# Optimization experiments

Measured on AMD Instinct MI355X. Metric: run time of the kernel, lower is better.

## Reference

```python
import jax, jax.numpy as jnp
import numpy as np

VOCAB = 50257
EMBED = 512
HEADS = 8
HEAD_DIM = EMBED // HEADS
WINDOW = 128
NUM_CLASS = 20
B, S = 4, 2048


def setup_inputs() -> dict:
    key = jax.random.key(0)
    ks = jax.random.split(key, 16)
    sc = 0.02
    inp = {
        'text': jax.random.randint(ks[0], (B, S), 0, VOCAB),
        'emb': jax.random.normal(ks[1], (VOCAB, EMBED), jnp.float32) * sc,
        'in_w': jax.random.normal(ks[2], (3 * EMBED, EMBED), jnp.float32) * sc,
        'in_b': jnp.zeros((3 * EMBED,), jnp.float32),
        'out_w': jax.random.normal(ks[3], (EMBED, EMBED), jnp.float32) * sc,
        'out_b': jnp.zeros((EMBED,), jnp.float32),
        'w1': jax.random.normal(ks[4], (512, EMBED), jnp.float32) * sc,
        'b1': jnp.zeros((512,), jnp.float32),
        'w2': jax.random.normal(ks[5], (256, 512), jnp.float32) * sc,
        'b2': jnp.zeros((256,), jnp.float32),
        'w3': jax.random.normal(ks[6], (128, 256), jnp.float32) * sc,
        'b3': jnp.zeros((128,), jnp.float32),
        'w4': jax.random.normal(ks[7], (NUM_CLASS, 128), jnp.float32) * sc,
        'b4': jnp.zeros((NUM_CLASS,), jnp.float32),
    }
    return inp


def _banded_mask(seq_len, window):
    i = jnp.arange(seq_len)[:, None]
    j = jnp.arange(seq_len)[None, :]
    allowed = jnp.abs(i - j) <= window  # band of width 2*window+1
    return jnp.where(allowed, 0.0, -jnp.inf).astype(jnp.float32)


def reference(text, emb, in_w, in_b, out_w, out_b, w1, b1, w2, b2, w3, b3, w4, b4):
    # Embedding lookup (dropout is identity in eval mode)
    x = emb[text]  # [B, S, E]
    b, s, e = x.shape

    # torch nn.MultiheadAttention: packed in_proj, scaling by 1/sqrt(head_dim)
    wq, wk, wv = in_w[:e], in_w[e:2 * e], in_w[2 * e:]
    bq, bk, bv = in_b[:e], in_b[e:2 * e], in_b[2 * e:]
    q = (x @ wq.T + bq).reshape(b, s, HEADS, HEAD_DIM)
    k = (x @ wk.T + bk).reshape(b, s, HEADS, HEAD_DIM)
    v = (x @ wv.T + bv).reshape(b, s, HEADS, HEAD_DIM)

    mask = _banded_mask(s, WINDOW)  # [S, S] additive, -inf outside band
    scores = jnp.einsum('bihd,bjhd->bhij', q, k) / jnp.sqrt(jnp.float32(HEAD_DIM))
    probs = jax.nn.softmax(scores + mask, axis=-1)  # [B, H, S, S]
    attn = jnp.einsum('bhij,bjhd->bihd', probs, v).reshape(b, s, e)
    attn = attn @ out_w.T + out_b  # [B, S, E]

    # max-pool over sequence
    ctx = jnp.max(attn, axis=1)  # [B, E]

    # MLP head with leaky_relu (negative_slope=0.01, torch default)
    h = jax.nn.leaky_relu(ctx @ w1.T + b1, 0.01)
    h = jax.nn.leaky_relu(h @ w2.T + b2, 0.01)
    h = jax.nn.leaky_relu(h @ w3.T + b3, 0.01)
    return h @ w4.T + b4  # [B, NUM_CLASS]
```

## Files before the change

### kernel.cpp

```cpp
#include <hip/hip_runtime.h>

typedef unsigned short u16;
typedef __attribute__((ext_vector_type(8))) short bf16x8;
typedef __attribute__((ext_vector_type(4))) float f32x4;

#define S_LEN 2048
#define EMBED 512
#define HEADS 8
#define HDIM 64
#define BATCH 4
#define TOKENS (BATCH * S_LEN)

__device__ __forceinline__ u16 f2bf(float f) {
  union { float f; unsigned u; } v;
  v.f = f;
  unsigned r = v.u + 0x7fffu + ((v.u >> 16) & 1u);
  return (u16)(r >> 16);
}

__device__ __forceinline__ void gl2lds16(const void* g, void* l) {
  __builtin_amdgcn_global_load_lds(
      (const __attribute__((address_space(1))) void*)g,
      (__attribute__((address_space(3))) void*)l, 16, 0, 0);
}

__global__ __launch_bounds__(256) void prep_kernel(
    const int* __restrict__ text, const float* __restrict__ emb,
    const float* __restrict__ in_w, const float* __restrict__ out_w,
    u16* __restrict__ Xb, u16* __restrict__ Wq, u16* __restrict__ Wo) {
  const int bid = blockIdx.x;
  const int tid = threadIdx.x;
  if (bid < 4096) {
    const int t = bid * 2 + (tid >> 7);
    const int c = (tid & 127) * 4;
    const size_t src = (size_t)text[t] * EMBED + c;
    const float4 v = *(const float4*)(emb + src);
    u16* dst = Xb + (size_t)t * EMBED + c;
    dst[0] = f2bf(v.x); dst[1] = f2bf(v.y); dst[2] = f2bf(v.z); dst[3] = f2bf(v.w);
  } else {
    const int idx4 = ((bid - 4096) * 256 + tid) * 4;
    const float* src;
    u16* dst;
    if (idx4 < 1536 * 512) { src = in_w + idx4; dst = Wq + idx4; }
    else { src = out_w + (idx4 - 1536 * 512); dst = Wo + (idx4 - 1536 * 512); }
    const float4 v = *(const float4*)src;
    dst[0] = f2bf(v.x); dst[1] = f2bf(v.y); dst[2] = f2bf(v.z); dst[3] = f2bf(v.w);
  }
}

__global__ __launch_bounds__(256, 3) void qkv_mfma(
    const u16* __restrict__ Xb, const u16* __restrict__ Wq,
    const float* __restrict__ in_b,
    u16* __restrict__ qg, u16* __restrict__ kg, u16* __restrict__ vt) {
  __shared__ u16 As[128 * 64];
  __shared__ u16 Bs[128 * 64];
  const int m0 = blockIdx.x * 128, n0 = blockIdx.y * 128;
  const int tid = threadIdx.x;
  const int w = tid >> 6, l = tid & 63, quad = l >> 4, ln = l & 15;
  const int rb = (w >> 1) * 64, cb = (w & 1) * 64;

  f32x4 acc[4][4] = {};

  for (int k0 = 0; k0 < EMBED; k0 += 64) {
#pragma unroll
    for (int it = 0; it < 4; ++it) {
      const int chunk = it * 256 + tid;
      const int row = chunk >> 3, cp = chunk & 7, c = cp ^ (row & 7);
      gl2lds16(Xb + (size_t)(m0 + row) * EMBED + k0 + c * 8, &As[chunk * 8]);
      gl2lds16(Wq + (size_t)(n0 + row) * EMBED + k0 + c * 8, &Bs[chunk * 8]);
    }
    __syncthreads();
#pragma unroll
    for (int s = 0; s < 2; ++s) {
      bf16x8 af[4], bf[4];
#pragma unroll
      for (int i = 0; i < 4; ++i) {
        const int r = rb + 16 * i + ln;
        af[i] = *(const bf16x8*)&As[r * 64 + (((s << 2) + quad) ^ (r & 7)) * 8];
      }
#pragma unroll
      for (int j = 0; j < 4; ++j) {
        const int n = cb + 16 * j + ln;
        bf[j] = *(const bf16x8*)&Bs[n * 64 + (((s << 2) + quad) ^ (n & 7)) * 8];
      }
#pragma unroll
      for (int i = 0; i < 4; ++i)
#pragma unroll
        for (int j = 0; j < 4; ++j)
          acc[i][j] = __builtin_amdgcn_mfma_f32_16x16x32_bf16(af[i], bf[j], acc[i][j], 0, 0, 0);
    }
    __syncthreads();
  }

#pragma unroll
  for (int j = 0; j < 4; ++j) {
    const int n = n0 + cb + 16 * j + ln;
    const float bias = in_b[n];
    const int sec = n >> 9, f = n & 511, h = f >> 6, d = f & 63;
#pragma unroll
    for (int i = 0; i < 4; ++i) {
#pragma unroll
      for (int r = 0; r < 4; ++r) {
        const int t = m0 + rb + 16 * i + quad * 4 + r;
        const int b = t >> 11, s = t & 2047;
        const float val = acc[i][j][r] + bias;
        if (sec == 0)
          qg[((size_t)((b * HEADS + h) * S_LEN + s)) * HDIM + d] = f2bf(val * 0.125f);
        else if (sec == 1)
          kg[((size_t)((b * HEADS + h) * S_LEN + s)) * HDIM + d] = f2bf(val);
        else
          vt[((size_t)((b * HEADS + h) * HDIM + d)) * S_LEN + s] = f2bf(val);
      }
    }
  }
}

__global__ __launch_bounds__(256, 3) void attn_mfma(
    const u16* __restrict__ qg, const u16* __restrict__ kg,
    const u16* __restrict__ vt, u16* __restrict__ attnb) {
  __shared__ u16 KV[320 * 64];
  __shared__ u16 Pb[4][16 * 40];
  const int bh = blockIdx.y;
  const int i0 = blockIdx.x * 64;
  const int jb = i0 - 128;
  const int tid = threadIdx.x;
  const int w = tid >> 6, l = tid & 63, quad = l >> 4, ln = l & 15;
  const int jlo = w, jhi = w + 16;

  const u16* qrow = qg + ((size_t)bh * S_LEN + i0 + w * 16 + ln) * HDIM;
  bf16x8 qf[2];
  qf[0] = *(const bf16x8*)(qrow + quad * 8);
  qf[1] = *(const bf16x8*)(qrow + 32 + quad * 8);

  const u16* kbase = kg + (size_t)bh * S_LEN * HDIM;
#pragma unroll
  for (int it = 0; it < 10; ++it) {
    const int chunk = it * 256 + tid;
    const int row = chunk >> 3, cp = chunk & 7, c = cp ^ (row & 7);
    int gj = jb + row;
    gj = gj < 0 ? 0 : (gj > S_LEN - 1 ? S_LEN - 1 : gj);
    gl2lds16(kbase + (size_t)gj * HDIM + c * 8, &KV[chunk * 8]);
  }
  __syncthreads();

  f32x4 sc[20] = {};
#pragma unroll
  for (int jt = 0; jt < 20; ++jt) {
    if (jt < jlo || jt > jhi) continue;
    const int r = jt * 16 + ln;
    const bf16x8 b0 = *(const bf16x8*)&KV[r * 64 + ((quad) ^ (r & 7)) * 8];
    const bf16x8 b1 = *(const bf16x8*)&KV[r * 64 + ((4 + quad) ^ (r & 7)) * 8];
    f32x4 a = {};
    a = __builtin_amdgcn_mfma_f32_16x16x32_bf16(qf[0], b0, a, 0, 0, 0);
    a = __builtin_amdgcn_mfma_f32_16x16x32_bf16(qf[1], b1, a, 0, 0, 0);
    sc[jt] = a;
  }
  __syncthreads();

  const u16* vbase = vt + (size_t)bh * HDIM * S_LEN;
#pragma unroll
  for (int it = 0; it < 10; ++it) {
    const int chunk = it * 256 + tid;
    const int row = chunk / 40, cp = chunk % 40, c = cp ^ (row & 7);
    int gc = jb + c * 8;
    gc = gc < 0 ? 0 : (gc > S_LEN - 8 ? S_LEN - 8 : gc);
    gl2lds16(vbase + (size_t)row * S_LEN + gc, &KV[chunk * 8]);
  }

  const int gibase = i0 + w * 16 + quad * 4;
  int lo[4], hi[4];
#pragma unroll
  for (int r = 0; r < 4; ++r) {
    const int gi = gibase + r;
    int lr = gi - 128, hr = gi + 128;
    lo[r] = lr < 0 ? 0 : lr;
    hi[r] = hr > S_LEN - 1 ? S_LEN - 1 : hr;
  }
  float mrow[4] = {-1e30f, -1e30f, -1e30f, -1e30f}, lrow[4];
#pragma unroll
  for (int jt = 0; jt < 20; ++jt) {
    if (jt < jlo || jt > jhi) continue;
    const int gj = jb + jt * 16 + ln;
#pragma unroll
    for (int r = 0; r < 4; ++r) {
      const bool valid = (gj >= lo[r]) && (gj <= hi[r]);
      const float v = valid ? sc[jt][r] : -1e30f;
      sc[jt][r] = v;
      mrow[r] = fmaxf(mrow[r], v);
    }
  }
#pragma unroll
  for (int r = 0; r < 4; ++r) {
    mrow[r] = fmaxf(mrow[r], __shfl_xor(mrow[r], 1));
    mrow[r] = fmaxf(mrow[r], __shfl_xor(mrow[r], 2));
    mrow[r] = fmaxf(mrow[r], __shfl_xor(mrow[r], 4));
    mrow[r] = fmaxf(mrow[r], __shfl_xor(mrow[r], 8));
    lrow[r] = 0.f;
  }
#pragma unroll
  for (int jt = 0; jt < 20; ++jt) {
    if (jt < jlo || jt > jhi) continue;
#pragma unroll
    for (int r = 0; r < 4; ++r) {
      const float e = __expf(sc[jt][r] - mrow[r]);
      sc[jt][r] = e;
      lrow[r] += e;
    }
  }
#pragma unroll
  for (int r = 0; r < 4; ++r) {
    lrow[r] += __shfl_xor(lrow[r], 1);
    lrow[r] += __shfl_xor(lrow[r], 2);
    lrow[r] += __shfl_xor(lrow[r], 4);
    lrow[r] += __shfl_xor(lrow[r], 8);
    lrow[r] = 1.0f / lrow[r];
  }

  __syncthreads();

  f32x4 oacc[4] = {};
  u16* pb = &Pb[w][0];
#pragma unroll
  for (int kt = 0; kt < 10; ++kt) {
    if (kt * 2 + 1 < jlo || kt * 2 > jhi) continue;
#pragma unroll
    for (int tt = 0; tt < 2; ++tt) {
      const int jt = kt * 2 + tt;
#pragma unroll
      for (int r = 0; r < 4; ++r)
        pb[(quad * 4 + r) * 40 + ln + 16 * tt] = f2bf(sc[jt][r]);
    }
    __asm__ volatile("" ::: "memory");
    const bf16x8 pa = *(const bf16x8*)&pb[ln * 40 + quad * 8];
#pragma unroll
    for (int dt = 0; dt < 4; ++dt) {
      const int d = dt * 16 + ln;
      const bf16x8 vb = *(const bf16x8*)&KV[d * 320 + ((kt * 4 + quad) ^ (d & 7)) * 8];
      oacc[dt] = __builtin_amdgcn_mfma_f32_16x16x32_bf16(pa, vb, oacc[dt], 0, 0, 0);
    }
  }

  const int b = bh >> 3, h = bh & 7;
#pragma unroll
  for (int dt = 0; dt < 4; ++dt) {
    const int d = h * HDIM + dt * 16 + ln;
#pragma unroll
    for (int r = 0; r < 4; ++r) {
      const int gi = i0 + w * 16 + quad * 4 + r;
      attnb[((size_t)(b * S_LEN + gi)) * EMBED + d] = f2bf(oacc[dt][r] * lrow[r]);
    }
  }
}

__global__ __launch_bounds__(256, 3) void outproj_mfma(
    const u16* __restrict__ attnb, const u16* __restrict__ Wo,
    const float* __restrict__ out_b, float* __restrict__ pmax) {
  __shared__ u16 As[128 * 64];
  __shared__ u16 Bs[64 * 64];
  __shared__ float red[4][32];
  const int m0 = blockIdx.x * 128, n0 = blockIdx.y * 64;
  const int tid = threadIdx.x;
  const int w = tid >> 6, l = tid & 63, quad = l >> 4, ln = l & 15;
  const int rb = (w >> 1) * 64, cb = (w & 1) * 32;

  f32x4 acc[4][2] = {};

  for (int k0 = 0; k0 < EMBED; k0 += 64) {
#pragma unroll
    for (int it = 0; it < 4; ++it) {
      const int chunk = it * 256 + tid;
      const int row = chunk >> 3, cp = chunk & 7, c = cp ^ (row & 7);
      gl2lds16(attnb + (size_t)(m0 + row) * EMBED + k0 + c * 8, &As[chunk * 8]);
    }
#pragma unroll
    for (int it = 0; it < 2; ++it) {
      const int chunk = it * 256 + tid;
      const int row = chunk >> 3, cp = chunk & 7, c = cp ^ (row & 7);
      gl2lds16(Wo + (size_t)(n0 + row) * EMBED + k0 + c * 8, &Bs[chunk * 8]);
    }
    __syncthreads();
#pragma unroll
    for (int s = 0; s < 2; ++s) {
      bf16x8 af[4], bf[2];
#pragma unroll
      for (int i = 0; i < 4; ++i) {
        const int r = rb + 16 * i + ln;
        af[i] = *(const bf16x8*)&As[r * 64 + (((s << 2) + quad) ^ (r & 7)) * 8];
      }
#pragma unroll
      for (int j = 0; j < 2; ++j) {
        const int n = cb + 16 * j + ln;
        bf[j] = *(const bf16x8*)&Bs[n * 64 + (((s << 2) + quad) ^ (n & 7)) * 8];
      }
#pragma unroll
      for (int i = 0; i < 4; ++i)
#pragma unroll
        for (int j = 0; j < 2; ++j)
          acc[i][j] = __builtin_amdgcn_mfma_f32_16x16x32_bf16(af[i], bf[j], acc[i][j], 0, 0, 0);
    }
    __syncthreads();
  }

  float cm[2];
#pragma unroll
  for (int j = 0; j < 2; ++j) {
    float m = -1e30f;
#pragma unroll
    for (int i = 0; i < 4; ++i)
#pragma unroll
      for (int r = 0; r < 4; ++r) m = fmaxf(m, acc[i][j][r]);
    m = fmaxf(m, __shfl_xor(m, 16));
    m = fmaxf(m, __shfl_xor(m, 32));
    cm[j] = m;
  }
  if (l < 16) {
#pragma unroll
    for (int j = 0; j < 2; ++j) red[w][16 * j + ln] = cm[j];
  }
  __syncthreads();
  if (tid < 64) {
    const int half = tid >> 5;
    const int cc = tid & 31;
    const float m = fmaxf(red[half][cc], red[half + 2][cc]);
    const int n = n0 + tid;
    const int b = m0 >> 11, stile = (m0 >> 7) & 15;
    pmax[(size_t)(b * 16 + stile) * EMBED + n] = m + out_b[n];
  }
}

__global__ __launch_bounds__(256) void mlp_ctx_l1(
    const float* __restrict__ pmax, const float* __restrict__ w1,
    const float* __restrict__ b1, float* __restrict__ h1g) {
  __shared__ float ctx[512];
  const int b = blockIdx.x >> 3, chunk = blockIdx.x & 7;
  const int tid = threadIdx.x;

  for (int e = tid; e < 512; e += 256) {
    float m = -1e30f;
#pragma unroll
    for (int t = 0; t < 16; ++t) m = fmaxf(m, pmax[(size_t)(b * 16 + t) * 512 + e]);
    ctx[e] = m;
  }
  __syncthreads();

  const int o = chunk * 64 + (tid >> 2), kq = tid & 3;
  float acc = 0.f;
  const float* wr = w1 + (size_t)o * 512 + kq * 128;
  const float* xr = ctx + kq * 128;
  for (int k = 0; k < 128; k += 4) {
    const float4 wv = *(const float4*)(wr + k);
    const float4 xv = *(const float4*)(xr + k);
    acc += wv.x * xv.x + wv.y * xv.y + wv.z * xv.z + wv.w * xv.w;
  }
  acc += __shfl_xor(acc, 1);
  acc += __shfl_xor(acc, 2);
  if (kq == 0) {
    const float a = acc + b1[o];
    h1g[b * 512 + o] = a > 0.f ? a : 0.01f * a;
  }
}

__global__ __launch_bounds__(256) void mlp_l2(
    const float* __restrict__ h1g, const float* __restrict__ w2,
    const float* __restrict__ b2, float* __restrict__ h2g) {
  __shared__ float xb[512];
  const int b = blockIdx.x >> 2, chunk = blockIdx.x & 3;
  const int tid = threadIdx.x;
  for (int e = tid; e < 512; e += 256) xb[e] = h1g[b * 512 + e];
  __syncthreads();

  const int o = chunk * 64 + (tid >> 2), kq = tid & 3;
  float acc = 0.f;
  const float* wr = w2 + (size_t)o * 512 + kq * 128;
  const float* xr = xb + kq * 128;
  for (int k = 0; k < 128; k += 4) {
    const float4 wv = *(const float4*)(wr + k);
    const float4 xv = *(const float4*)(xr + k);
    acc += wv.x * xv.x + wv.y * xv.y + wv.z * xv.z + wv.w * xv.w;
  }
  acc += __shfl_xor(acc, 1);
  acc += __shfl_xor(acc, 2);
  if (kq == 0) {
    const float a = acc + b2[o];
    h2g[b * 256 + o] = a > 0.f ? a : 0.01f * a;
  }
}

__global__ __launch_bounds__(256) void mlp_l34(
    const float* __restrict__ h2g,
    const float* __restrict__ w3, const float* __restrict__ b3,
    const float* __restrict__ w4, const float* __restrict__ b4,
    float* __restrict__ out) {
  __shared__ float xb[256], h3[128];
  const int b = blockIdx.x, tid = threadIdx.x;
  if (tid < 256) xb[tid] = h2g[b * 256 + tid];
  __syncthreads();

  {
    const int o = tid >> 1, kh = tid & 1;
    float acc = 0.f;
    const float* wr = w3 + (size_t)o * 256 + kh * 128;
    const float* xr = xb + kh * 128;
    for (int k = 0; k < 128; k += 4) {
      const float4 wv = *(const float4*)(wr + k);
      const float4 xv = *(const float4*)(xr + k);
      acc += wv.x * xv.x + wv.y * xv.y + wv.z * xv.z + wv.w * xv.w;
    }
    acc += __shfl_xor(acc, 1);
    if (kh == 0) { const float a = acc + b3[o]; h3[o] = a > 0.f ? a : 0.01f * a; }
  }
  __syncthreads();

  if (tid < 160) {
    const int o = tid >> 3, ks = tid & 7;
    const float* wr = w4 + (size_t)o * 128 + ks * 16;
    const float* xr = h3 + ks * 16;
    float acc = 0.f;
    for (int k = 0; k < 16; k += 4) {
      const float4 wv = *(const float4*)(wr + k);
      const float4 xv = *(const float4*)(xr + k);
      acc += wv.x * xv.x + wv.y * xv.y + wv.z * xv.z + wv.w * xv.w;
    }
    acc += __shfl_xor(acc, 1);
    acc += __shfl_xor(acc, 2);
    acc += __shfl_xor(acc, 4);
    if (ks == 0) out[b * 20 + o] = acc + b4[o];
  }
}

extern "C" void kernel_launch(void* const* d_in, const int* in_sizes, int n_in,
                              void* d_out, int out_size, void* d_ws, size_t ws_size,
                              hipStream_t stream) {
  (void)in_sizes; (void)n_in; (void)out_size; (void)ws_size;
  const int*   text  = (const int*)d_in[0];
  const float* emb   = (const float*)d_in[1];
  const float* in_w  = (const float*)d_in[2];
  const float* in_b  = (const float*)d_in[3];
  const float* out_w = (const float*)d_in[4];
  const float* out_b = (const float*)d_in[5];
  const float* w1 = (const float*)d_in[6];
  const float* b1 = (const float*)d_in[7];
  const float* w2 = (const float*)d_in[8];
  const float* b2 = (const float*)d_in[9];
  const float* w3 = (const float*)d_in[10];
  const float* b3 = (const float*)d_in[11];
  const float* w4 = (const float*)d_in[12];
  const float* b4 = (const float*)d_in[13];

  char* ws = (char*)d_ws;
  u16* Xb   = (u16*)(ws);
  u16* Wq   = (u16*)(ws + 8388608);
  u16* Wo   = (u16*)(ws + 9961472);
  u16* qg   = (u16*)(ws + 10485760);
  u16* kg   = (u16*)(ws + 18874368);
  u16* vt   = (u16*)(ws + 27262976);
  u16* attn = (u16*)(ws + 35651584);
  float* pmax = (float*)(ws + 44040192);
  float* h1g  = (float*)(ws + 44171264);
  float* h2g  = (float*)(ws + 44179456);

  prep_kernel<<<5120, 256, 0, stream>>>(text, emb, in_w, out_w, Xb, Wq, Wo);
  qkv_mfma<<<dim3(64, 12), 256, 0, stream>>>(Xb, Wq, in_b, qg, kg, vt);
  attn_mfma<<<dim3(32, 32), 256, 0, stream>>>(qg, kg, vt, attn);
  outproj_mfma<<<dim3(64, 8), 256, 0, stream>>>(attn, Wo, out_b, pmax);
  mlp_ctx_l1<<<32, 256, 0, stream>>>(pmax, w1, b1, h1g);
  mlp_l2<<<16, 256, 0, stream>>>(h1g, w2, b2, h2g);
  mlp_l34<<<4, 256, 0, stream>>>(h2g, w3, b3, w4, b4, (float*)d_out);
}
```

Before: 238.2 us.

## Fuse seq max-pool via atomicMax, remap attention blocks, widen MLP grids

The out-projection now reduces its per-tile column maxima straight into a per-batch context vector using atomicMax on order-preserving unsigned keys. This removes the intermediate partial-max buffer and the reduction loop in the first MLP layer, and prep_kernel gains an extra block that zeroes the context buffer. The attention launch becomes a 1D grid with a remapped block index, likely aimed at XCD/L2 locality. The MLP layers 1 and 2 launch more blocks, each computing fewer outputs with 16 lanes per output, to raise parallelism on these small latency-bound kernels.

```diff
diff --git a/kernel.cpp b/kernel.cpp
--- a/kernel.cpp
+++ b/kernel.cpp
@@ -18,6 +18,15 @@
   return (u16)(r >> 16);
 }
 
+__device__ __forceinline__ unsigned fkey(float f) {
+  unsigned u = __float_as_uint(f);
+  return (u & 0x80000000u) ? ~u : (u | 0x80000000u);
+}
+__device__ __forceinline__ float funkey(unsigned k) {
+  unsigned u = (k & 0x80000000u) ? (k ^ 0x80000000u) : ~k;
+  return __uint_as_float(u);
+}
+
 __device__ __forceinline__ void gl2lds16(const void* g, void* l) {
   __builtin_amdgcn_global_load_lds(
       (const __attribute__((address_space(1))) void*)g,
@@ -27,7 +36,8 @@
 __global__ __launch_bounds__(256) void prep_kernel(
     const int* __restrict__ text, const float* __restrict__ emb,
     const float* __restrict__ in_w, const float* __restrict__ out_w,
-    u16* __restrict__ Xb, u16* __restrict__ Wq, u16* __restrict__ Wo) {
+    u16* __restrict__ Xb, u16* __restrict__ Wq, u16* __restrict__ Wo,
+    unsigned* __restrict__ ctxi) {
   const int bid = blockIdx.x;
   const int tid = threadIdx.x;
   if (bid < 4096) {
@@ -37,7 +47,7 @@
     const float4 v = *(const float4*)(emb + src);
     u16* dst = Xb + (size_t)t * EMBED + c;
     dst[0] = f2bf(v.x); dst[1] = f2bf(v.y); dst[2] = f2bf(v.z); dst[3] = f2bf(v.w);
-  } else {
+  } else if (bid < 5120) {
     const int idx4 = ((bid - 4096) * 256 + tid) * 4;
     const float* src;
     u16* dst;
@@ -45,6 +55,8 @@
     else { src = out_w + (idx4 - 1536 * 512); dst = Wo + (idx4 - 1536 * 512); }
     const float4 v = *(const float4*)src;
     dst[0] = f2bf(v.x); dst[1] = f2bf(v.y); dst[2] = f2bf(v.z); dst[3] = f2bf(v.w);
+  } else {
+    for (int i = tid; i < BATCH * EMBED; i += 256) ctxi[i] = 0u;
   }
 }
 
@@ -120,8 +132,10 @@
     const u16* __restrict__ vt, u16* __restrict__ attnb) {
   __shared__ u16 KV[320 * 64];
   __shared__ u16 Pb[4][16 * 40];
-  const int bh = blockIdx.y;
-  const int i0 = blockIdx.x * 64;
+  const int lid = blockIdx.x;
+  const int nid = (lid & 7) * 128 + (lid >> 3);
+  const int bh = nid >> 5;
+  const int i0 = (nid & 31) * 64;
   const int jb = i0 - 128;
   const int tid = threadIdx.x;
   const int w = tid >> 6, l = tid & 63, quad = l >> 4, ln = l & 15;
@@ -254,7 +268,7 @@
 
 __global__ __launch_bounds__(256, 3) void outproj_mfma(
     const u16* __restrict__ attnb, const u16* __restrict__ Wo,
-    const float* __restrict__ out_b, float* __restrict__ pmax) {
+    const float* __restrict__ out_b, unsigned* __restrict__ ctxi) {
   __shared__ u16 As[128 * 64];
   __shared__ u16 Bs[64 * 64];
   __shared__ float red[4][32];
@@ -323,38 +337,35 @@
     const int cc = tid & 31;
     const float m = fmaxf(red[half][cc], red[half + 2][cc]);
     const int n = n0 + tid;
-    const int b = m0 >> 11, stile = (m0 >> 7) & 15;
-    pmax[(size_t)(b * 16 + stile) * EMBED + n] = m + out_b[n];
-  }
-}
-
-__global__ __launch_bounds__(256) void mlp_ctx_l1(
-    const float* __restrict__ pmax, const float* __restrict__ w1,
+    const int b = m0 >> 11;
+    atomicMax(&ctxi[b * EMBED + n], fkey(m + out_b[n]));
+  }
+}
+
+__global__ __launch_bounds__(256) void mlp_l1(
+    const unsigned* __restrict__ ctxi, const float* __restrict__ w1,
     const float* __restrict__ b1, float* __restrict__ h1g) {
   __shared__ float ctx[512];
-  const int b = blockIdx.x >> 3, chunk = blockIdx.x & 7;
-  const int tid = threadIdx.x;
-
-  for (int e = tid; e < 512; e += 256) {
-    float m = -1e30f;
-#pragma unroll
-    for (int t = 0; t < 16; ++t) m = fmaxf(m, pmax[(size_t)(b * 16 + t) * 512 + e]);
-    ctx[e] = m;
-  }
-  __syncthreads();
-
-  const int o = chunk * 64 + (tid >> 2), kq = tid & 3;
+  const int b = blockIdx.x >> 5, chunk = blockIdx.x & 31;
+  const int tid = threadIdx.x;
+  for (int e = tid; e < 512; e += 256) ctx[e] = funkey(ctxi[b * 512 + e]);
+  __syncthreads();
+
+  const int og = tid >> 4, ln = tid & 15;
+  const int o = chunk * 16 + og;
+  const float4* wv = (const float4*)(w1 + (size_t)o * 512 + ln * 32);
+  const float4* xv = (const float4*)(ctx + ln * 32);
   float acc = 0.f;
-  const float* wr = w1 + (size_t)o * 512 + kq * 128;
-  const float* xr = ctx + kq * 128;
-  for (int k = 0; k < 128; k += 4) {
-    const float4 wv = *(const float4*)(wr + k);
-    const float4 xv = *(const float4*)(xr + k);
-    acc += wv.x * xv.x + wv.y * xv.y + wv.z * xv.z + wv.w * xv.w;
+#pragma unroll
+  for (int k = 0; k < 8; ++k) {
+    const float4 a = wv[k], x = xv[k];
+    acc += a.x * x.x + a.y * x.y + a.z * x.z + a.w * x.w;
   }
   acc += __shfl_xor(acc, 1);
   acc += __shfl_xor(acc, 2);
-  if (kq == 0) {
+  acc += __shfl_xor(acc, 4);
+  acc += __shfl_xor(acc, 8);
+  if (ln == 0) {
     const float a = acc + b1[o];
     h1g[b * 512 + o] = a > 0.f ? a : 0.01f * a;
   }
@@ -364,23 +375,26 @@
     const float* __restrict__ h1g, const float* __restrict__ w2,
     const float* __restrict__ b2, float* __restrict__ h2g) {
   __shared__ float xb[512];
-  const int b = blockIdx.x >> 2, chunk = blockIdx.x & 3;
+  const int b = blockIdx.x >> 4, chunk = blockIdx.x & 15;
   const int tid = threadIdx.x;
   for (int e = tid; e < 512; e += 256) xb[e] = h1g[b * 512 + e];
   __syncthreads();
 
-  const int o = chunk * 64 + (tid >> 2), kq = tid & 3;
+  const int og = tid >> 4, ln = tid & 15;
+  const int o = chunk * 16 + og;
+  const float4* wv = (const float4*)(w2 + (size_t)o * 512 + ln * 32);
+  const float4* xv = (const float4*)(xb + ln * 32);
   float acc = 0.f;
-  const float* wr = w2 + (size_t)o * 512 + kq * 128;
-  const float* xr = xb + kq * 128;
-  for (int k = 0; k < 128; k += 4) {
-    const float4 wv = *(const float4*)(wr + k);
-    const float4 xv = *(const float4*)(xr + k);
-    acc += wv.x * xv.x + wv.y * xv.y + wv.z * xv.z + wv.w * xv.w;
+#pragma unroll
+  for (int k = 0; k < 8; ++k) {
+    const float4 a = wv[k], x = xv[k];
+    acc += a.x * x.x + a.y * x.y + a.z * x.z + a.w * x.w;
   }
   acc += __shfl_xor(acc, 1);
   acc += __shfl_xor(acc, 2);
-  if (kq == 0) {
+  acc += __shfl_xor(acc, 4);
+  acc += __shfl_xor(acc, 8);
+  if (ln == 0) {
     const float a = acc + b2[o];
     h2g[b * 256 + o] = a > 0.f ? a : 0.01f * a;
   }
@@ -455,15 +469,15 @@
   u16* kg   = (u16*)(ws + 18874368);
   u16* vt   = (u16*)(ws + 27262976);
   u16* attn = (u16*)(ws + 35651584);
-  float* pmax = (float*)(ws + 44040192);
-  float* h1g  = (float*)(ws + 44171264);
-  float* h2g  = (float*)(ws + 44179456);
-
-  prep_kernel<<<5120, 256, 0, stream>>>(text, emb, in_w, out_w, Xb, Wq, Wo);
+  unsigned* ctxi = (unsigned*)(ws + 44040192);
+  float* h1g  = (float*)(ws + 44048384);
+  float* h2g  = (float*)(ws + 44056576);
+
+  prep_kernel<<<5121, 256, 0, stream>>>(text, emb, in_w, out_w, Xb, Wq, Wo, ctxi);
   qkv_mfma<<<dim3(64, 12), 256, 0, stream>>>(Xb, Wq, in_b, qg, kg, vt);
-  attn_mfma<<<dim3(32, 32), 256, 0, stream>>>(qg, kg, vt, attn);
-  outproj_mfma<<<dim3(64, 8), 256, 0, stream>>>(attn, Wo, out_b, pmax);
-  mlp_ctx_l1<<<32, 256, 0, stream>>>(pmax, w1, b1, h1g);
-  mlp_l2<<<16, 256, 0, stream>>>(h1g, w2, b2, h2g);
+  attn_mfma<<<1024, 256, 0, stream>>>(qg, kg, vt, attn);
+  outproj_mfma<<<dim3(64, 8), 256, 0, stream>>>(attn, Wo, out_b, ctxi);
+  mlp_l1<<<128, 256, 0, stream>>>(ctxi, w1, b1, h1g);
+  mlp_l2<<<64, 256, 0, stream>>>(h1g, w2, b2, h2g);
   mlp_l34<<<4, 256, 0, stream>>>(h2g, w3, b3, w4, b4, (float*)d_out);
 }
```

Result: faster. 228.3 us (-4.1%).
